# Optimization experiments

Measured on AMD Instinct MI355X. Metric: run time of the kernel, lower is better.

Reference implementation:

```python
import jax, jax.numpy as jnp
import numpy as np

WS = 7       # window_size
SHIFT = 3    # shift_size
HEADS = 3
EPS = 1e-5


def _rel_index():
    # (2, N) coords of a WS x WS window, then pairwise relative offsets -> flat table index
    coords = np.stack(np.meshgrid(np.arange(WS), np.arange(WS), indexing='ij')).reshape(2, -1)
    rel = (coords[:, :, None] - coords[:, None, :]).transpose(1, 2, 0) + (WS - 1)  # (N,N,2)
    return jnp.asarray(rel[..., 0] * (2 * WS - 1) + rel[..., 1])  # (N,N) int


def _layernorm(x, g, b):
    mu = jnp.mean(x, axis=-1, keepdims=True)
    var = jnp.mean(jnp.square(x - mu), axis=-1, keepdims=True)
    return (x - mu) * jax.lax.rsqrt(var + EPS) * g + b


def setup_inputs() -> dict:
    key = jax.random.key(0)
    ks = jax.random.split(key, 6)
    C, HID = 96, 384
    s = 0.02
    return {
        'x': jax.random.normal(ks[0], (8, C, 224, 224), jnp.float32),
        'norm1_g': jnp.ones((C,), jnp.float32),
        'norm1_b': jnp.zeros((C,), jnp.float32),
        'qkv_w': jax.random.normal(ks[1], (C, 3 * C), jnp.float32) * s,
        'qkv_b': jnp.zeros((3 * C,), jnp.float32),
        'proj_w': jax.random.normal(ks[2], (C, C), jnp.float32) * s,
        'proj_b': jnp.zeros((C,), jnp.float32),
        'rel_bias_table': jax.random.normal(ks[3], ((2 * WS - 1) ** 2, HEADS), jnp.float32) * s,
        'norm2_g': jnp.ones((C,), jnp.float32),
        'norm2_b': jnp.zeros((C,), jnp.float32),
        'fc1_w': jax.random.normal(ks[4], (C, HID), jnp.float32) * s,
        'fc1_b': jnp.zeros((HID,), jnp.float32),
        'fc2_w': jax.random.normal(ks[5], (HID, C), jnp.float32) * s,
        'fc2_b': jnp.zeros((C,), jnp.float32),
    }


def reference(x, norm1_g, norm1_b, qkv_w, qkv_b, proj_w, proj_b,
              rel_bias_table, norm2_g, norm2_b, fc1_w, fc1_b, fc2_w, fc2_b):
    B, C, H, W = x.shape
    N = WS * WS
    dh = C // HEADS

    # norm1 over channels (tokens = flattened spatial)
    xt = x.reshape(B, C, H * W).transpose(0, 2, 1)          # (B, L, C)
    xn = _layernorm(xt, norm1_g, norm1_b)
    xs = xn.transpose(0, 2, 1).reshape(B, C, H, W)
    # H, W divisible by WS -> pad is a no-op; cyclic shift
    xs = jnp.roll(xs, (-SHIFT, -SHIFT), axis=(2, 3))

    # window partition -> (B*nW, N, C)
    xw = xs.reshape(B, C, H // WS, WS, W // WS, WS)
    xw = xw.transpose(0, 2, 4, 3, 5, 1).reshape(-1, N, C)

    # window attention with relative position bias (no shift mask, per source)
    Bw = xw.shape[0]
    qkv = (xw @ qkv_w + qkv_b).reshape(Bw, N, 3, HEADS, dh).transpose(2, 0, 3, 1, 4)
    q, k, v = qkv[0], qkv[1], qkv[2]                        # (Bw, h, N, dh)
    attn = jnp.einsum('bhnd,bhmd->bhnm', q, k) * (dh ** -0.5)
    bias = rel_bias_table[_rel_index().reshape(-1)].reshape(N, N, HEADS).transpose(2, 0, 1)
    attn = jax.nn.softmax(attn + bias, axis=-1)
    out = jnp.einsum('bhnm,bhmd->bhnd', attn, v).transpose(0, 2, 1, 3).reshape(Bw, N, C)
    out = out @ proj_w + proj_b

    # window reverse + unshift
    xr = out.reshape(B, H // WS, W // WS, WS, WS, C)
    xr = xr.transpose(0, 5, 1, 3, 2, 4).reshape(B, C, H, W)
    xr = jnp.roll(xr, (SHIFT, SHIFT), axis=(2, 3))

    x = x + xr                                              # residual 1

    # MLP branch with norm2 (exact GELU, matching torch nn.GELU default)
    xt = x.reshape(B, C, H * W).transpose(0, 2, 1)
    xn = _layernorm(xt, norm2_g, norm2_b)
    h = jax.nn.gelu(xn @ fc1_w + fc1_b, approximate=False)
    h = h @ fc2_w + fc2_b
    return x + h.transpose(0, 2, 1).reshape(B, C, H, W)
```

## Files before the change

kernel.cpp:

```cpp
#include <hip/hip_runtime.h>
#include <hip/hip_bf16.h>
#include <math.h>

#define WSZ 7
#define NTOK 49
#define CH 96
#define HIMG 224
#define WIMG 224
#define HWIMG (224*224)
#define SHIFT_ 3
#define HID 384

typedef __attribute__((ext_vector_type(8))) short bf16x8;
typedef __attribute__((ext_vector_type(4))) float f32x4;
typedef unsigned int u32;
typedef unsigned short u16;

__device__ __forceinline__ u32 pk2(float a, float b) {
    u16 ua = __builtin_bit_cast(u16, __float2bfloat16(a));
    u16 ub = __builtin_bit_cast(u16, __float2bfloat16(b));
    return (u32)ua | ((u32)ub << 16);
}
__device__ __forceinline__ float bflo(u32 u) { return __builtin_bit_cast(float, u << 16); }

union FragU { u32 w[4]; bf16x8 v; };

__device__ __forceinline__ bf16x8 regroup(u32 t0w0, u32 t0w1, u32 t1w0, u32 t1w1, int lane) {
    int sl0 = (lane & 15) + ((lane & 16) << 1);
    int sl1 = sl0 + 16;
    u32 x0 = (u32)__shfl((int)t0w0, sl0);
    u32 y0 = (u32)__shfl((int)t1w0, sl0);
    u32 x1 = (u32)__shfl((int)t0w1, sl0);
    u32 y1 = (u32)__shfl((int)t1w1, sl0);
    u32 x2 = (u32)__shfl((int)t0w0, sl1);
    u32 y2 = (u32)__shfl((int)t1w0, sl1);
    u32 x3 = (u32)__shfl((int)t0w1, sl1);
    u32 y3 = (u32)__shfl((int)t1w1, sl1);
    bool lo = lane < 32;
    FragU f;
    f.w[0] = lo ? x0 : y0;
    f.w[1] = lo ? x1 : y1;
    f.w[2] = lo ? x2 : y2;
    f.w[3] = lo ? x3 : y3;
    return f.v;
}

__device__ __forceinline__ float gelu_f(float x) {
    float x2 = x * x;
    float t  = x * (1.5957691216057308f + 0.07135481283587191f * x2);
    float e  = __expf(t);
    float r  = __builtin_amdgcn_rcpf(e + 1.0f);
    return x - x * r;
}

__global__ __launch_bounds__(256) void prep_kernel(
    const float* __restrict__ w1, const float* __restrict__ w2,
    const float* __restrict__ pw, const float* __restrict__ qw,
    __hip_bfloat16* __restrict__ ws, int n)
{
    int i = blockIdx.x * 256 + threadIdx.x;
    if (i >= n) return;
    float val = 0.f;
    if (i < 81920) {
        int ch = i / 20480, r = i - ch * 20480;
        int half = r / 10240;
        int rr = r - half * 10240;
        if (rr < 9984) {
            int row = rr / 104, col = rr - row * 104;
            if (col < 96)
                val = (half == 0) ? w1[col * HID + ch * 96 + row]
                                  : w2[(size_t)(ch * 96 + col) * CH + row];
        }
    } else if (i < 92160) {
        int r = i - 81920;
        if (r < 9984) {
            int row = r / 104, col = r - row * 104;
            if (col < 96) val = pw[col * CH + row];
        }
    } else {
        int j = i - 92160;
        int hh = j / 9984, rr = j - hh * 9984;
        int dp = rr / 104, c = rr - dp * 104;
        if (c < 96) {
            int colW = (dp < 32) ? (hh * 32 + dp)
                     : (dp < 64) ? (96 + hh * 32 + dp - 32)
                                 : (192 + hh * 32 + dp - 64);
            val = qw[c * 288 + colW];
        }
    }
    ws[i] = __float2bfloat16(val);
}

__global__ __launch_bounds__(256) void attn2_kernel(
    const float* __restrict__ x,
    const float* __restrict__ g1, const float* __restrict__ b1,
    const __hip_bfloat16* __restrict__ wsW,
    const float* __restrict__ qkv_b, const float* __restrict__ pb,
    const float* __restrict__ btab,
    __hip_bfloat16* __restrict__ projout)
{
    const int tid  = threadIdx.x;
    const int lane = tid & 63;
    const int wv   = tid >> 6;
    const int l15  = lane & 15;
    const int g    = lane >> 4;
    const int bi   = blockIdx.x;
    const int b    = bi >> 8;
    const int wh   = (bi >> 3) & 31;
    const int ww0  = (bi & 7) * 4;
    const int ww   = ww0 + wv;

    __shared__ float btabL[507];
    __shared__ __align__(16) char uniA[43008];

    __hip_bfloat16 (*xsb)[7][32] = (__hip_bfloat16(*)[7][32])uniA;
    __hip_bfloat16 (*vT)[72] = (__hip_bfloat16(*)[72])(uniA + wv * 4608);
    u32* prS = (u32*)(uniA + wv * 4608);

    for (int idx = tid; idx < 507; idx += 256) btabL[idx] = btab[idx];

    const int colBase = ww0 * 7 + 3;
    const int cA  = colBase & ~3;
    const int cb4 = cA >> 2;
    const int a0  = colBase & 3;
    #pragma unroll
    for (int k = 0; k < 21; ++k) {
        int idx = tid + 256 * k;
        int c = idx / 56, rem = idx - c * 56;
        int r = rem >> 3, cf = rem & 7;
        int gr = wh * 7 + 3 + r; if (gr >= HIMG) gr -= HIMG;
        int g4 = cb4 + cf; if (g4 >= 56) g4 -= 56;
        float4 v = *(const float4*)(x + ((size_t)(b * CH + c) * HIMG + gr) * WIMG + g4 * 4);
        uint2 pk;
        pk.x = pk2(v.x, v.y);
        pk.y = pk2(v.z, v.w);
        *(uint2*)&xsb[c][r][cf * 4] = pk;
    }
    __syncthreads();

    bf16x8 xB[4][3];
    #pragma unroll
    for (int it = 0; it < 4; ++it) {
        int i = it * 16 + l15;
        bool real = i < NTOK;
        int yi = i / 7, xi = i - yi * 7;
        int sc = a0 + wv * 7 + xi;
        float raw[24];
        float s0 = 0.f, s1 = 0.f;
        #pragma unroll
        for (int ks = 0; ks < 3; ++ks)
            #pragma unroll
            for (int t = 0; t < 8; ++t) {
                int c = ks * 32 + g * 8 + t;
                float v = real ? __bfloat162float(xsb[c][yi][sc]) : 0.f;
                raw[ks * 8 + t] = v; s0 += v; s1 += v * v;
            }
        s0 += __shfl_xor(s0, 16); s0 += __shfl_xor(s0, 32);
        s1 += __shfl_xor(s1, 16); s1 += __shfl_xor(s1, 32);
        float mu = s0 * (1.0f / CH);
        float rstd = rsqrtf(s1 * (1.0f / CH) - mu * mu + 1e-5f);
        #pragma unroll
        for (int ks = 0; ks < 3; ++ks)
            #pragma unroll
            for (int t = 0; t < 8; ++t) {
                int c = ks * 32 + g * 8 + t;
                float xv = real ? ((raw[ks * 8 + t] - mu) * rstd * g1[c] + b1[c]) : 0.f;
                xB[it][ks][t] = (short)__builtin_bit_cast(u16, __float2bfloat16(xv));
            }
    }
    __syncthreads();

    const float scale = 0.17677669529663687f;
    bf16x8 aoB[3][4];

    for (int h = 0; h < 3; ++h) {
        const __hip_bfloat16* qkvTg = wsW + 92160 + h * 9984;

        float qb[2][4], kb[2][4], vb[2][4];
        #pragma unroll
        for (int dt = 0; dt < 2; ++dt)
            #pragma unroll
            for (int r = 0; r < 4; ++r) {
                int d = h * 32 + dt * 16 + g * 4 + r;
                qb[dt][r] = qkv_b[d];
                kb[dt][r] = qkv_b[96 + d];
                vb[dt][r] = qkv_b[192 + d];
            }

        u32 Qpk[2][4][2];
        #pragma unroll
        for (int dt = 0; dt < 2; ++dt) {
            const __hip_bfloat16* wr = qkvTg + (dt * 16 + l15) * 104 + g * 8;
            bf16x8 a0f = *(const bf16x8*)(wr);
            bf16x8 a1f = *(const bf16x8*)(wr + 32);
            bf16x8 a2f = *(const bf16x8*)(wr + 64);
            #pragma unroll
            for (int it = 0; it < 4; ++it) {
                f32x4 c4 = {0.f, 0.f, 0.f, 0.f};
                c4 = __builtin_amdgcn_mfma_f32_16x16x32_bf16(a0f, xB[it][0], c4, 0, 0, 0);
                c4 = __builtin_amdgcn_mfma_f32_16x16x32_bf16(a1f, xB[it][1], c4, 0, 0, 0);
                c4 = __builtin_amdgcn_mfma_f32_16x16x32_bf16(a2f, xB[it][2], c4, 0, 0, 0);
                Qpk[dt][it][0] = pk2(c4[0] + qb[dt][0], c4[1] + qb[dt][1]);
                Qpk[dt][it][1] = pk2(c4[2] + qb[dt][2], c4[3] + qb[dt][3]);
            }
        }
        bf16x8 QB[4];
        #pragma unroll
        for (int it = 0; it < 4; ++it)
            QB[it] = regroup(Qpk[0][it][0], Qpk[0][it][1], Qpk[1][it][0], Qpk[1][it][1], lane);

        u32 Kpk[2][4][2];
        #pragma unroll
        for (int dt = 0; dt < 2; ++dt) {
            const __hip_bfloat16* wr = qkvTg + (32 + dt * 16 + l15) * 104 + g * 8;
            bf16x8 a0f = *(const bf16x8*)(wr);
            bf16x8 a1f = *(const bf16x8*)(wr + 32);
            bf16x8 a2f = *(const bf16x8*)(wr + 64);
            #pragma unroll
            for (int it = 0; it < 4; ++it) {
                f32x4 c4 = {0.f, 0.f, 0.f, 0.f};
                c4 = __builtin_amdgcn_mfma_f32_16x16x32_bf16(a0f, xB[it][0], c4, 0, 0, 0);
                c4 = __builtin_amdgcn_mfma_f32_16x16x32_bf16(a1f, xB[it][1], c4, 0, 0, 0);
                c4 = __builtin_amdgcn_mfma_f32_16x16x32_bf16(a2f, xB[it][2], c4, 0, 0, 0);
                Kpk[dt][it][0] = pk2(c4[0] + kb[dt][0], c4[1] + kb[dt][1]);
                Kpk[dt][it][1] = pk2(c4[2] + kb[dt][2], c4[3] + kb[dt][3]);
            }
        }
        bf16x8 KA[4];
        #pragma unroll
        for (int it = 0; it < 4; ++it)
            KA[it] = regroup(Kpk[0][it][0], Kpk[0][it][1], Kpk[1][it][0], Kpk[1][it][1], lane);

        #pragma unroll
        for (int dt = 0; dt < 2; ++dt) {
            const __hip_bfloat16* wr = qkvTg + (64 + dt * 16 + l15) * 104 + g * 8;
            bf16x8 a0f = *(const bf16x8*)(wr);
            bf16x8 a1f = *(const bf16x8*)(wr + 32);
            bf16x8 a2f = *(const bf16x8*)(wr + 64);
            #pragma unroll
            for (int it = 0; it < 4; ++it) {
                f32x4 c4 = {0.f, 0.f, 0.f, 0.f};
                c4 = __builtin_amdgcn_mfma_f32_16x16x32_bf16(a0f, xB[it][0], c4, 0, 0, 0);
                c4 = __builtin_amdgcn_mfma_f32_16x16x32_bf16(a1f, xB[it][1], c4, 0, 0, 0);
                c4 = __builtin_amdgcn_mfma_f32_16x16x32_bf16(a2f, xB[it][2], c4, 0, 0, 0);
                #pragma unroll
                for (int r = 0; r < 4; ++r)
                    vT[dt * 16 + g * 4 + r][it * 16 + l15] = __float2bfloat16(c4[r] + vb[dt][r]);
            }
        }
        bf16x8 VBf[2][2];
        #pragma unroll
        for (int dt = 0; dt < 2; ++dt)
            #pragma unroll
            for (int ks = 0; ks < 2; ++ks)
                VBf[dt][ks] = *(const bf16x8*)&vT[dt * 16 + l15][ks * 32 + g * 8];

        #pragma unroll
        for (int it = 0; it < 4; ++it) {
            f32x4 SC[4];
            #pragma unroll
            for (int jt = 0; jt < 4; ++jt) {
                f32x4 z = {0.f, 0.f, 0.f, 0.f};
                SC[jt] = __builtin_amdgcn_mfma_f32_16x16x32_bf16(KA[jt], QB[it], z, 0, 0, 0);
            }
            int i = it * 16 + l15;
            int yi = i / 7, xi = i - yi * 7;
            float p[16];
            float m = -1e30f;
            #pragma unroll
            for (int jt = 0; jt < 4; ++jt)
                #pragma unroll
                for (int r = 0; r < 4; ++r) {
                    int j = jt * 16 + g * 4 + r;
                    int yj = j / 7, xj = j - yj * 7;
                    int rel = (yi - yj + 6) * 13 + (xi - xj + 6);
                    rel = rel < 0 ? 0 : (rel > 168 ? 168 : rel);
                    float s = (j < NTOK) ? (SC[jt][r] * scale + btabL[rel * 3 + h]) : -1e30f;
                    p[jt * 4 + r] = s;
                    m = fmaxf(m, s);
                }
            m = fmaxf(m, __shfl_xor(m, 16));
            m = fmaxf(m, __shfl_xor(m, 32));
            float sum = 0.f;
            #pragma unroll
            for (int q = 0; q < 16; ++q) { float e = __expf(p[q] - m); p[q] = e; sum += e; }
            sum += __shfl_xor(sum, 16);
            sum += __shfl_xor(sum, 32);
            float inv = 1.f / sum;
            u32 Ppk[4][2];
            #pragma unroll
            for (int jt = 0; jt < 4; ++jt) {
                Ppk[jt][0] = pk2(p[jt * 4 + 0] * inv, p[jt * 4 + 1] * inv);
                Ppk[jt][1] = pk2(p[jt * 4 + 2] * inv, p[jt * 4 + 3] * inv);
            }
            bf16x8 PA0 = regroup(Ppk[0][0], Ppk[0][1], Ppk[1][0], Ppk[1][1], lane);
            bf16x8 PA1 = regroup(Ppk[2][0], Ppk[2][1], Ppk[3][0], Ppk[3][1], lane);
            u32 opk[2][2];
            #pragma unroll
            for (int dt = 0; dt < 2; ++dt) {
                f32x4 o = {0.f, 0.f, 0.f, 0.f};
                o = __builtin_amdgcn_mfma_f32_16x16x32_bf16(PA0, VBf[dt][0], o, 0, 0, 0);
                o = __builtin_amdgcn_mfma_f32_16x16x32_bf16(PA1, VBf[dt][1], o, 0, 0, 0);
                opk[dt][0] = pk2(o[0], o[1]);
                opk[dt][1] = pk2(o[2], o[3]);
            }
            aoB[h][it] = regroup(opk[0][0], opk[0][1], opk[1][0], opk[1][1], lane);
        }
    }

    const __hip_bfloat16* pwTg = wsW + 81920;
    for (int it = 0; it < 4; ++it) {
        #pragma unroll
        for (int mt = 0; mt < 6; ++mt) {
            const __hip_bfloat16* wr = pwTg + (mt * 16 + l15) * 104 + g * 8;
            f32x4 cp = {0.f, 0.f, 0.f, 0.f};
            #pragma unroll
            for (int ks = 0; ks < 3; ++ks) {
                bf16x8 af = *(const bf16x8*)(wr + ks * 32);
                cp = __builtin_amdgcn_mfma_f32_16x16x32_bf16(af, aoB[ks][it], cp, 0, 0, 0);
            }
            float v0 = cp[0] + pb[mt * 16 + g * 4 + 0];
            float v1 = cp[1] + pb[mt * 16 + g * 4 + 1];
            float v2 = cp[2] + pb[mt * 16 + g * 4 + 2];
            float v3 = cp[3] + pb[mt * 16 + g * 4 + 3];
            prS[l15 * 52 + mt * 8 + g * 2 + 0] = pk2(v0, v1);
            prS[l15 * 52 + mt * 8 + g * 2 + 1] = pk2(v2, v3);
        }
        #pragma unroll
        for (int s = 0; s < 3; ++s) {
            int chunk = lane + 64 * s;
            int row = chunk / 12, q = chunk - row * 12;
            int tok = it * 16 + row;
            if (tok < NTOK) {
                int yi = tok / 7, xi = tok - yi * 7;
                int hh = wh * 7 + yi + SHIFT_; if (hh >= HIMG) hh -= HIMG;
                int wp = ww * 7 + xi + SHIFT_; if (wp >= WIMG) wp -= WIMG;
                float4 val = *(const float4*)((const char*)prS + row * 208 + q * 16);
                *(float4*)(projout + ((size_t)b * HWIMG + hh * WIMG + wp) * 96 + q * 8) = val;
            }
        }
    }
}

#define LDSTG(p0, p1, p2, s) { const float4* _s = wsrc + (s) * 1280; \
    p0 = _s[tid]; p1 = _s[tid + 512]; if (tid < 256) p2 = _s[tid + 1024]; }
#define WRSTG(p0, p1, p2, off) { float4* _d = (float4*)(SB + (off)); \
    _d[tid] = p0; _d[tid + 512] = p1; if (tid < 256) _d[tid + 1024] = p2; }

__global__ __launch_bounds__(512, 4) void mlp2_kernel(
    const float* __restrict__ x, const __hip_bfloat16* __restrict__ projout,
    const float* __restrict__ g2, const float* __restrict__ b2,
    const float* __restrict__ bb1, const float* __restrict__ bb2,
    const __hip_bfloat16* __restrict__ wsW,
    float* __restrict__ out)
{
    const int tid = threadIdx.x;
    const int lane = tid & 63, wv = tid >> 6;
    const int l15 = lane & 15, g = lane >> 4;
    const int b = blockIdx.x / 392;
    const int hw0 = (blockIdx.x % 392) * 128;
    const int tok = wv * 16 + l15;

    __shared__ __align__(16) char SB[50688];
    __shared__ float bb1S[HID];

    __hip_bfloat16 (*xnS)[104] = (__hip_bfloat16(*)[104])SB;
    __hip_bfloat16 (*wT0)[104] = (__hip_bfloat16(*)[104])SB;
    __hip_bfloat16 (*wT1)[104] = (__hip_bfloat16(*)[104])(SB + 20480);
    float* ob = (float*)SB;

    const float4* wsrc = (const float4*)wsW;
    float4 ra0, ra1, ra2, rb0, rb1, rb2;

    LDSTG(ra0, ra1, ra2, 0);

    #pragma unroll
    for (int s = 0; s < 3; ++s) {
        int chunk = tid + 512 * s;
        int row = chunk / 12, q = chunk - row * 12;
        *(float4*)&xnS[row][q * 8] =
            *(const float4*)(projout + ((size_t)b * HWIMG + hw0 + row) * 96 + q * 8);
    }
    for (int idx = tid; idx < HID; idx += 512) bb1S[idx] = bb1[idx];
    __syncthreads();

    float xr[24];
    float s0 = 0.f, s1 = 0.f;
    bf16x8 pf[3];
    #pragma unroll
    for (int ks = 0; ks < 3; ++ks)
        pf[ks] = *(const bf16x8*)&xnS[tok][ks * 32 + g * 8];
    const float* xb = x + (size_t)(b * CH) * HWIMG + hw0 + tok;
    #pragma unroll
    for (int ks = 0; ks < 3; ++ks)
        #pragma unroll
        for (int j = 0; j < 8; ++j) {
            int c = ks * 32 + g * 8 + j;
            float xv = xb[(size_t)c * HWIMG];
            float v = xv + bflo((u32)(u16)pf[ks][j]);
            xr[ks * 8 + j] = v; s0 += v; s1 += v * v;
        }
    s0 += __shfl_xor(s0, 16); s0 += __shfl_xor(s0, 32);
    s1 += __shfl_xor(s1, 16); s1 += __shfl_xor(s1, 32);
    float mu = s0 * (1.0f / CH);
    float rstd = rsqrtf(s1 * (1.0f / CH) - mu * mu + 1e-5f);

    bf16x8 xbf[3];
    #pragma unroll
    for (int ks = 0; ks < 3; ++ks) {
        float nv[8];
        #pragma unroll
        for (int j = 0; j < 8; ++j) {
            int c = ks * 32 + g * 8 + j;
            nv[j] = (xr[ks * 8 + j] - mu) * rstd * g2[c] + b2[c];
        }
        FragU f;
        f.w[0] = pk2(nv[0], nv[1]); f.w[1] = pk2(nv[2], nv[3]);
        f.w[2] = pk2(nv[4], nv[5]); f.w[3] = pk2(nv[6], nv[7]);
        xbf[ks] = f.v;
    }
    __syncthreads();

    WRSTG(ra0, ra1, ra2, 0);
    LDSTG(rb0, rb1, rb2, 1);
    __syncthreads();

    f32x4 acc[6];
    #pragma unroll
    for (int mt = 0; mt < 6; ++mt) {
        #pragma unroll
        for (int r = 0; r < 4; ++r) acc[mt][r] = bb2[mt * 16 + g * 4 + r];
    }

    #pragma unroll
    for (int ch = 0; ch < 4; ++ch) {
        u32 hpk[6][2];
        #pragma unroll
        for (int mt = 0; mt < 6; ++mt) {
            f32x4 f = {0.f, 0.f, 0.f, 0.f};
            #pragma unroll
            for (int ks = 0; ks < 3; ++ks) {
                bf16x8 af = *(const bf16x8*)&wT0[mt * 16 + l15][ks * 32 + g * 8];
                f = __builtin_amdgcn_mfma_f32_16x16x32_bf16(af, xbf[ks], f, 0, 0, 0);
            }
            float gl[4];
            #pragma unroll
            for (int r = 0; r < 4; ++r) {
                float a = f[r] + bb1S[ch * 96 + mt * 16 + g * 4 + r];
                gl[r] = gelu_f(a);
            }
            hpk[mt][0] = pk2(gl[0], gl[1]);
            hpk[mt][1] = pk2(gl[2], gl[3]);
        }
        WRSTG(rb0, rb1, rb2, 20480);
        __syncthreads();
        if (ch < 3) LDSTG(ra0, ra1, ra2, 2 * ch + 2);

        bf16x8 hf[3];
        hf[0] = regroup(hpk[0][0], hpk[0][1], hpk[1][0], hpk[1][1], lane);
        hf[1] = regroup(hpk[2][0], hpk[2][1], hpk[3][0], hpk[3][1], lane);
        hf[2] = regroup(hpk[4][0], hpk[4][1], hpk[5][0], hpk[5][1], lane);
        #pragma unroll
        for (int mt = 0; mt < 6; ++mt) {
            #pragma unroll
            for (int ks = 0; ks < 3; ++ks) {
                bf16x8 af = *(const bf16x8*)&wT1[mt * 16 + l15][ks * 32 + g * 8];
                acc[mt] = __builtin_amdgcn_mfma_f32_16x16x32_bf16(af, hf[ks], acc[mt], 0, 0, 0);
            }
        }
        if (ch < 3) WRSTG(ra0, ra1, ra2, 0);
        __syncthreads();
        if (ch < 3) LDSTG(rb0, rb1, rb2, 2 * ch + 3);
    }

    #pragma unroll
    for (int ks = 0; ks < 3; ++ks)
        #pragma unroll
        for (int j = 0; j < 8; ++j)
            ob[tok * 99 + ks * 32 + g * 8 + j] = xr[ks * 8 + j];
    __syncthreads();
    #pragma unroll
    for (int mt = 0; mt < 6; ++mt)
        #pragma unroll
        for (int r = 0; r < 4; ++r)
            ob[tok * 99 + mt * 16 + g * 4 + r] += acc[mt][r];
    __syncthreads();
    #pragma unroll
    for (int k = 0; k < 24; ++k) {
        int idx = tid + 512 * k;
        int c = idx >> 7, t = idx & 127;
        out[(size_t)(b * CH + c) * HWIMG + hw0 + t] = ob[t * 99 + c];
    }
}

__global__ __launch_bounds__(256) void attn_mfma_kernel(
    const float* __restrict__ x,
    const float* __restrict__ g1, const float* __restrict__ b1,
    const float* __restrict__ qkv_w, const float* __restrict__ qkv_b,
    const float* __restrict__ btab,
    float* __restrict__ ao)
{
    const int tid  = threadIdx.x;
    const int lane = tid & 63;
    const int wv   = tid >> 6;
    const int l15  = lane & 15;
    const int g    = lane >> 4;
    const int wid  = blockIdx.x * 4 + wv;
    const int b    = wid >> 10;
    const int wh   = (wid >> 5) & 31;
    const int ww   = wid & 31;

    __shared__ __align__(16) __hip_bfloat16 wT[96][104];
    __shared__ float btabL[507];
    __shared__ __align__(16) __hip_bfloat16 vT[4][32][72];
    __shared__ __align__(16) __hip_bfloat16 Ob[4][64][36];

    int to_h = 0, to_w = 0;
    if (lane < NTOK) {
        int yl = lane / 7, xl = lane - yl * 7;
        to_h = wh * 7 + yl + SHIFT_; if (to_h >= HIMG) to_h -= HIMG;
        to_w = ww * 7 + xl + SHIFT_; if (to_w >= WIMG) to_w -= WIMG;
    }

    bf16x8 xB[4][3];
    #pragma unroll
    for (int it = 0; it < 4; ++it) {
        int i = it * 16 + l15;
        bool real = i < NTOK;
        int yi = i / 7, xi = i - yi * 7;
        int hh = wh * 7 + yi + SHIFT_; if (hh >= HIMG) hh -= HIMG;
        int wp = ww * 7 + xi + SHIFT_; if (wp >= WIMG) wp -= WIMG;
        float raw[24];
        float s0 = 0.f, s1 = 0.f;
        #pragma unroll
        for (int ks = 0; ks < 3; ++ks)
            #pragma unroll
            for (int t = 0; t < 8; ++t) {
                int c = ks * 32 + g * 8 + t;
                float v = real ? x[((size_t)(b * CH + c) * HIMG + hh) * WIMG + wp] : 0.f;
                raw[ks * 8 + t] = v; s0 += v; s1 += v * v;
            }
        s0 += __shfl_xor(s0, 16); s0 += __shfl_xor(s0, 32);
        s1 += __shfl_xor(s1, 16); s1 += __shfl_xor(s1, 32);
        float mu = s0 * (1.0f / CH);
        float rstd = rsqrtf(s1 * (1.0f / CH) - mu * mu + 1e-5f);
        #pragma unroll
        for (int ks = 0; ks < 3; ++ks)
            #pragma unroll
            for (int t = 0; t < 8; ++t) {
                int c = ks * 32 + g * 8 + t;
                float xv = real ? ((raw[ks * 8 + t] - mu) * rstd * g1[c] + b1[c]) : 0.f;
                xB[it][ks][t] = (short)__builtin_bit_cast(u16, __float2bfloat16(xv));
            }
    }

    const float scale = 0.17677669529663687f;

    for (int h = 0; h < 3; ++h) {
        __syncthreads();
        for (int idx = tid; idx < 96 * 96; idx += 256) {
            int c = idx / 96, dp = idx - c * 96;
            int col = (dp < 32) ? (h * 32 + dp) : (dp < 64) ? (96 + h * 32 + dp - 32)
                                                            : (192 + h * 32 + dp - 64);
            wT[dp][c] = __float2bfloat16(qkv_w[c * 288 + col]);
        }
        if (h == 0)
            for (int idx = tid; idx < 507; idx += 256) btabL[idx] = btab[idx];
        __syncthreads();

        float qb[2][4], kb[2][4], vb[2][4];
        #pragma unroll
        for (int dt = 0; dt < 2; ++dt)
            #pragma unroll
            for (int r = 0; r < 4; ++r) {
                int d = h * 32 + dt * 16 + g * 4 + r;
                qb[dt][r] = qkv_b[d];
                kb[dt][r] = qkv_b[96 + d];
                vb[dt][r] = qkv_b[192 + d];
            }

        u32 Qpk[2][4][2];
        #pragma unroll
        for (int dt = 0; dt < 2; ++dt) {
            bf16x8 a0 = *(const bf16x8*)&wT[dt * 16 + l15][0 * 32 + g * 8];
            bf16x8 a1 = *(const bf16x8*)&wT[dt * 16 + l15][1 * 32 + g * 8];
            bf16x8 a2 = *(const bf16x8*)&wT[dt * 16 + l15][2 * 32 + g * 8];
            #pragma unroll
            for (int it = 0; it < 4; ++it) {
                f32x4 c4 = {0.f, 0.f, 0.f, 0.f};
                c4 = __builtin_amdgcn_mfma_f32_16x16x32_bf16(a0, xB[it][0], c4, 0, 0, 0);
                c4 = __builtin_amdgcn_mfma_f32_16x16x32_bf16(a1, xB[it][1], c4, 0, 0, 0);
                c4 = __builtin_amdgcn_mfma_f32_16x16x32_bf16(a2, xB[it][2], c4, 0, 0, 0);
                Qpk[dt][it][0] = pk2(c4[0] + qb[dt][0], c4[1] + qb[dt][1]);
                Qpk[dt][it][1] = pk2(c4[2] + qb[dt][2], c4[3] + qb[dt][3]);
            }
        }
        bf16x8 QB[4];
        #pragma unroll
        for (int it = 0; it < 4; ++it)
            QB[it] = regroup(Qpk[0][it][0], Qpk[0][it][1], Qpk[1][it][0], Qpk[1][it][1], lane);

        u32 Kpk[2][4][2];
        #pragma unroll
        for (int dt = 0; dt < 2; ++dt) {
            bf16x8 a0 = *(const bf16x8*)&wT[32 + dt * 16 + l15][0 * 32 + g * 8];
            bf16x8 a1 = *(const bf16x8*)&wT[32 + dt * 16 + l15][1 * 32 + g * 8];
            bf16x8 a2 = *(const bf16x8*)&wT[32 + dt * 16 + l15][2 * 32 + g * 8];
            #pragma unroll
            for (int it = 0; it < 4; ++it) {
                f32x4 c4 = {0.f, 0.f, 0.f, 0.f};
                c4 = __builtin_amdgcn_mfma_f32_16x16x32_bf16(a0, xB[it][0], c4, 0, 0, 0);
                c4 = __builtin_amdgcn_mfma_f32_16x16x32_bf16(a1, xB[it][1], c4, 0, 0, 0);
                c4 = __builtin_amdgcn_mfma_f32_16x16x32_bf16(a2, xB[it][2], c4, 0, 0, 0);
                Kpk[dt][it][0] = pk2(c4[0] + kb[dt][0], c4[1] + kb[dt][1]);
                Kpk[dt][it][1] = pk2(c4[2] + kb[dt][2], c4[3] + kb[dt][3]);
            }
        }
        bf16x8 KA[4];
        #pragma unroll
        for (int it = 0; it < 4; ++it)
            KA[it] = regroup(Kpk[0][it][0], Kpk[0][it][1], Kpk[1][it][0], Kpk[1][it][1], lane);

        #pragma unroll
        for (int dt = 0; dt < 2; ++dt) {
            bf16x8 a0 = *(const bf16x8*)&wT[64 + dt * 16 + l15][0 * 32 + g * 8];
            bf16x8 a1 = *(const bf16x8*)&wT[64 + dt * 16 + l15][1 * 32 + g * 8];
            bf16x8 a2 = *(const bf16x8*)&wT[64 + dt * 16 + l15][2 * 32 + g * 8];
            #pragma unroll
            for (int it = 0; it < 4; ++it) {
                f32x4 c4 = {0.f, 0.f, 0.f, 0.f};
                c4 = __builtin_amdgcn_mfma_f32_16x16x32_bf16(a0, xB[it][0], c4, 0, 0, 0);
                c4 = __builtin_amdgcn_mfma_f32_16x16x32_bf16(a1, xB[it][1], c4, 0, 0, 0);
                c4 = __builtin_amdgcn_mfma_f32_16x16x32_bf16(a2, xB[it][2], c4, 0, 0, 0);
                #pragma unroll
                for (int r = 0; r < 4; ++r)
                    vT[wv][dt * 16 + g * 4 + r][it * 16 + l15] = __float2bfloat16(c4[r] + vb[dt][r]);
            }
        }
        bf16x8 VBf[2][2];
        #pragma unroll
        for (int dt = 0; dt < 2; ++dt)
            #pragma unroll
            for (int ks = 0; ks < 2; ++ks)
                VBf[dt][ks] = *(const bf16x8*)&vT[wv][dt * 16 + l15][ks * 32 + g * 8];

        #pragma unroll
        for (int it = 0; it < 4; ++it) {
            f32x4 SC[4];
            #pragma unroll
            for (int jt = 0; jt < 4; ++jt) {
                f32x4 z = {0.f, 0.f, 0.f, 0.f};
                SC[jt] = __builtin_amdgcn_mfma_f32_16x16x32_bf16(KA[jt], QB[it], z, 0, 0, 0);
            }
            int i = it * 16 + l15;
            int yi = i / 7, xi = i - yi * 7;
            float p[16];
            float m = -1e30f;
            #pragma unroll
            for (int jt = 0; jt < 4; ++jt)
                #pragma unroll
                for (int r = 0; r < 4; ++r) {
                    int j = jt * 16 + g * 4 + r;
                    int yj = j / 7, xj = j - yj * 7;
                    int rel = (yi - yj + 6) * 13 + (xi - xj + 6);
                    rel = rel < 0 ? 0 : (rel > 168 ? 168 : rel);
                    float s = (j < NTOK) ? (SC[jt][r] * scale + btabL[rel * 3 + h]) : -1e30f;
                    p[jt * 4 + r] = s;
                    m = fmaxf(m, s);
                }
            m = fmaxf(m, __shfl_xor(m, 16));
            m = fmaxf(m, __shfl_xor(m, 32));
            float sum = 0.f;
            #pragma unroll
            for (int q = 0; q < 16; ++q) { float e = __expf(p[q] - m); p[q] = e; sum += e; }
            sum += __shfl_xor(sum, 16);
            sum += __shfl_xor(sum, 32);
            float inv = 1.f / sum;
            u32 Ppk[4][2];
            #pragma unroll
            for (int jt = 0; jt < 4; ++jt) {
                Ppk[jt][0] = pk2(p[jt * 4 + 0] * inv, p[jt * 4 + 1] * inv);
                Ppk[jt][1] = pk2(p[jt * 4 + 2] * inv, p[jt * 4 + 3] * inv);
            }
            bf16x8 PA0 = regroup(Ppk[0][0], Ppk[0][1], Ppk[1][0], Ppk[1][1], lane);
            bf16x8 PA1 = regroup(Ppk[2][0], Ppk[2][1], Ppk[3][0], Ppk[3][1], lane);
            #pragma unroll
            for (int dt = 0; dt < 2; ++dt) {
                f32x4 o = {0.f, 0.f, 0.f, 0.f};
                o = __builtin_amdgcn_mfma_f32_16x16x32_bf16(PA0, VBf[dt][0], o, 0, 0, 0);
                o = __builtin_amdgcn_mfma_f32_16x16x32_bf16(PA1, VBf[dt][1], o, 0, 0, 0);
                #pragma unroll
                for (int r = 0; r < 4; ++r)
                    Ob[wv][it * 16 + g * 4 + r][dt * 16 + l15] = __float2bfloat16(o[r]);
            }
        }

        if (lane < NTOK) {
            #pragma unroll 8
            for (int ch = 0; ch < 32; ++ch)
                ao[((size_t)(b * CH + h * 32 + ch) * HIMG + to_h) * WIMG + to_w] =
                    __bfloat162float(Ob[wv][lane][ch]);
        }
    }
}

__global__ __launch_bounds__(512, 4) void fuse2_kernel(
    const float* __restrict__ x, const float* ao,
    const float* __restrict__ pw, const float* __restrict__ pb,
    const float* __restrict__ g2, const float* __restrict__ b2,
    const float* __restrict__ w1, const float* __restrict__ bb1,
    const float* __restrict__ w2, const float* __restrict__ bb2,
    const __hip_bfloat16* __restrict__ wsW, int useWs,
    float* out)
{
    const int tid = threadIdx.x;
    const int lane = tid & 63, wv = tid >> 6;
    const int l15 = lane & 15, g = lane >> 4;
    const int b = blockIdx.x / 392;
    const int hw0 = (blockIdx.x % 392) * 128;
    const int m0 = wv * 16;
    const int t = tid & 127;
    const int c0 = tid >> 7;

    __shared__ __align__(16) char WREG[46592];
    __shared__ __align__(16) __hip_bfloat16 xnS[128][104];
    __shared__ float part0[4][128], part1[4][128];
    __shared__ float muS[128], rsS[128];
    __shared__ float bb1S[HID];

    __hip_bfloat16 (*pwT)[104]   = (__hip_bfloat16(*)[104])WREG;
    __hip_bfloat16 (*projS)[104] = (__hip_bfloat16(*)[104])(WREG + 19968);
    __hip_bfloat16 (*w1T)[104]   = (__hip_bfloat16(*)[104])WREG;
    __hip_bfloat16 (*w2T)[104]   = (__hip_bfloat16(*)[104])(WREG + 20480);
    __hip_bfloat16 (*obuf)[104]  = (__hip_bfloat16(*)[104])WREG;

    float xreg[24];

    for (int idx = tid, k = 0; idx < 96 * 128; idx += 512, ++k) {
        int c = idx >> 7, tt = idx & 127;
        size_t gi = (size_t)(b * CH + c) * HWIMG + hw0 + tt;
        xreg[k] = x[gi];
        xnS[tt][c] = __float2bfloat16(ao[gi]);
    }
    if (useWs) {
        const float4* src = (const float4*)wsW + 10240;
        float4* dst = (float4*)WREG;
        for (int i = tid; i < 1280; i += 512) dst[i] = src[i];
    } else {
        for (int idx = tid; idx < 96 * 96; idx += 512) {
            int c = idx / 96, oc = idx - c * 96;
            pwT[oc][c] = __float2bfloat16(pw[c * 96 + oc]);
        }
    }
    for (int idx = tid; idx < HID; idx += 512) bb1S[idx] = bb1[idx];
    __syncthreads();

    {
        bf16x8 bfr[3];
        #pragma unroll
        for (int ks = 0; ks < 3; ++ks)
            bfr[ks] = *(const bf16x8*)&xnS[m0 + l15][ks * 32 + g * 8];
        #pragma unroll
        for (int mt = 0; mt < 6; ++mt) {
            f32x4 cp = {0.f, 0.f, 0.f, 0.f};
            #pragma unroll
            for (int ks = 0; ks < 3; ++ks) {
                bf16x8 af = *(const bf16x8*)&pwT[mt * 16 + l15][ks * 32 + g * 8];
                cp = __builtin_amdgcn_mfma_f32_16x16x32_bf16(af, bfr[ks], cp, 0, 0, 0);
            }
            #pragma unroll
            for (int r = 0; r < 4; ++r) {
                int oc = mt * 16 + g * 4 + r;
                projS[m0 + l15][oc] = __float2bfloat16(cp[r] + pb[oc]);
            }
        }
    }
    __syncthreads();

    {
        float s0 = 0.f, s1 = 0.f;
        #pragma unroll
        for (int k = 0; k < 24; ++k) {
            int c = c0 + 4 * k;
            float v = xreg[k] + __bfloat162float(projS[t][c]);
            xreg[k] = v; s0 += v; s1 += v * v;
        }
        part0[c0][t] = s0; part1[c0][t] = s1;
    }
    __syncthreads();
    if (tid < 128) {
        float s0 = part0[0][tid] + part0[1][tid] + part0[2][tid] + part0[3][tid];
        float s1 = part1[0][tid] + part1[1][tid] + part1[2][tid] + part1[3][tid];
        float m = s0 * (1.0f / CH);
        muS[tid] = m;
        rsS[tid] = rsqrtf(s1 * (1.0f / CH) - m * m + 1e-5f);
    }
    __syncthreads();
    #pragma unroll
    for (int k = 0; k < 24; ++k) {
        int c = c0 + 4 * k;
        xnS[t][c] = __float2bfloat16((xreg[k] - muS[t]) * rsS[t] * g2[c] + b2[c]);
    }
    __syncthreads();

    bf16x8 xbf[3];
    #pragma unroll
    for (int ks = 0; ks < 3; ++ks)
        xbf[ks] = *(const bf16x8*)&xnS[m0 + l15][ks * 32 + g * 8];

    f32x4 acc[6];
    #pragma unroll
    for (int mt = 0; mt < 6; ++mt)
        #pragma unroll
        for (int r = 0; r < 4; ++r)
            acc[mt][r] = bb2[mt * 16 + g * 4 + r];

    for (int ch = 0; ch < 4; ++ch) {
        if (useWs) {
            const float4* src = (const float4*)wsW + (size_t)ch * 2560;
            float4* dst = (float4*)WREG;
            #pragma unroll
            for (int i = tid; i < 2560; i += 512) dst[i] = src[i];
        } else {
            for (int idx = tid; idx < 2 * 96 * 96; idx += 512) {
                if (idx < 9216) {
                    int kk = idx / 96, n = idx - kk * 96;
                    w1T[n][kk] = __float2bfloat16(w1[kk * HID + ch * 96 + n]);
                } else {
                    int j = idx - 9216;
                    int kk = j / 96, n = j - kk * 96;
                    w2T[n][kk] = __float2bfloat16(w2[(size_t)(ch * 96 + kk) * CH + n]);
                }
            }
        }
        __syncthreads();

        u32 hpk[6][2];
        #pragma unroll
        for (int mt = 0; mt < 6; ++mt) {
            f32x4 f = {0.f, 0.f, 0.f, 0.f};
            #pragma unroll
            for (int ks = 0; ks < 3; ++ks) {
                bf16x8 af = *(const bf16x8*)&w1T[mt * 16 + l15][ks * 32 + g * 8];
                f = __builtin_amdgcn_mfma_f32_16x16x32_bf16(af, xbf[ks], f, 0, 0, 0);
            }
            float gl[4];
            #pragma unroll
            for (int r = 0; r < 4; ++r) {
                float a = f[r] + bb1S[ch * 96 + mt * 16 + g * 4 + r];
                gl[r] = gelu_f(a);
            }
            hpk[mt][0] = pk2(gl[0], gl[1]);
            hpk[mt][1] = pk2(gl[2], gl[3]);
        }
        bf16x8 hf[3];
        hf[0] = regroup(hpk[0][0], hpk[0][1], hpk[1][0], hpk[1][1], lane);
        hf[1] = regroup(hpk[2][0], hpk[2][1], hpk[3][0], hpk[3][1], lane);
        hf[2] = regroup(hpk[4][0], hpk[4][1], hpk[5][0], hpk[5][1], lane);

        #pragma unroll
        for (int mt = 0; mt < 6; ++mt)
            #pragma unroll
            for (int ks = 0; ks < 3; ++ks) {
                bf16x8 af = *(const bf16x8*)&w2T[mt * 16 + l15][ks * 32 + g * 8];
                acc[mt] = __builtin_amdgcn_mfma_f32_16x16x32_bf16(af, hf[ks], acc[mt], 0, 0, 0);
            }
        __syncthreads();
    }

    #pragma unroll
    for (int mt = 0; mt < 6; ++mt)
        #pragma unroll
        for (int r = 0; r < 4; ++r)
            obuf[m0 + l15][mt * 16 + g * 4 + r] = __float2bfloat16(acc[mt][r]);
    __syncthreads();
    #pragma unroll
    for (int k = 0; k < 24; ++k) {
        int c = c0 + 4 * k;
        out[(size_t)(b * CH + c) * HWIMG + hw0 + t] = xreg[k] + __bfloat162float(obuf[t][c]);
    }
}

extern "C" void kernel_launch(void* const* d_in, const int* in_sizes, int n_in,
                              void* d_out, int out_size, void* d_ws, size_t ws_size,
                              hipStream_t stream) {
    const float* x    = (const float*)d_in[0];
    const float* n1g  = (const float*)d_in[1];
    const float* n1b  = (const float*)d_in[2];
    const float* qkvw = (const float*)d_in[3];
    const float* qkvb = (const float*)d_in[4];
    const float* pw   = (const float*)d_in[5];
    const float* pbv  = (const float*)d_in[6];
    const float* bt   = (const float*)d_in[7];
    const float* n2g  = (const float*)d_in[8];
    const float* n2b  = (const float*)d_in[9];
    const float* f1w  = (const float*)d_in[10];
    const float* f1b  = (const float*)d_in[11];
    const float* f2w  = (const float*)d_in[12];
    const float* f2b  = (const float*)d_in[13];
    float* out = (float*)d_out;

    const size_t FULL_NEED = 262144ull + 77070336ull;
    if (ws_size >= FULL_NEED) {
        __hip_bfloat16* wsW = (__hip_bfloat16*)d_ws;
        __hip_bfloat16* projout = (__hip_bfloat16*)((char*)d_ws + 262144);
        prep_kernel<<<477, 256, 0, stream>>>(f1w, f2w, pw, qkvw, wsW, 122112);
        attn2_kernel<<<2048, 256, 0, stream>>>(x, n1g, n1b, wsW, qkvb, pbv, bt, projout);
        mlp2_kernel<<<3136, 512, 0, stream>>>(x, projout, n2g, n2b, f1b, f2b, wsW, out);
    } else {
        int useWs = (ws_size >= 184320) ? 1 : 0;
        if (useWs)
            prep_kernel<<<360, 256, 0, stream>>>(f1w, f2w, pw, qkvw, (__hip_bfloat16*)d_ws, 92160);
        attn_mfma_kernel<<<2048, 256, 0, stream>>>(x, n1g, n1b, qkvw, qkvb, bt, out);
        fuse2_kernel<<<3136, 512, 0, stream>>>(x, out, pw, pbv, n2g, n2b, f1w, f1b, f2w, f2b,
                                               (const __hip_bfloat16*)d_ws, useWs, out);
    }
}
```

Baseline: 405.5 us.

## Stage input in 32-channel slabs to cut LDS and precompute bias indices

Input staging into shared memory now goes through a 32-channel slab, loaded three times in sequence, instead of holding all 96 channels at once. This shrinks LDS use so that, together with launch_bounds(256,4), more blocks can be resident per CU. LayerNorm statistics are accumulated across the slabs, and normalization is applied afterwards to packed bf16 fragments using vectorized gamma/beta loads. Relative-position bias indexing is simplified by precomputing packed per-lane token offsets and padding the bias table with -1e30 sentinels, which removes divisions and masking from the softmax loop. The cost is extra barriers and a small extra rounding step, since raw values are stored as bf16 before normalization.

Measured after the change: 477.1 us. +17.7%, slower.

```diff
diff --git a/kernel.cpp b/kernel.cpp
--- a/kernel.cpp
+++ b/kernel.cpp
@@ -22,6 +22,7 @@
     return (u32)ua | ((u32)ub << 16);
 }
 __device__ __forceinline__ float bflo(u32 u) { return __builtin_bit_cast(float, u << 16); }
+__device__ __forceinline__ float bfhi(u32 u) { return __builtin_bit_cast(float, u & 0xFFFF0000u); }
 
 union FragU { u32 w[4]; bf16x8 v; };
 
@@ -91,7 +92,7 @@
     ws[i] = __float2bfloat16(val);
 }
 
-__global__ __launch_bounds__(256) void attn2_kernel(
+__global__ __launch_bounds__(256, 4) void attn2_kernel(
     const float* __restrict__ x,
     const float* __restrict__ g1, const float* __restrict__ b1,
     const __hip_bfloat16* __restrict__ wsW,
@@ -110,65 +111,108 @@
     const int ww0  = (bi & 7) * 4;
     const int ww   = ww0 + wv;
 
-    __shared__ float btabL[507];
-    __shared__ __align__(16) char uniA[43008];
-
-    __hip_bfloat16 (*xsb)[7][32] = (__hip_bfloat16(*)[7][32])uniA;
-    __hip_bfloat16 (*vT)[72] = (__hip_bfloat16(*)[72])(uniA + wv * 4608);
-    u32* prS = (u32*)(uniA + wv * 4608);
-
-    for (int idx = tid; idx < 507; idx += 256) btabL[idx] = btab[idx];
+    __shared__ float btabL[512];
+    __shared__ __align__(16) __hip_bfloat16 slab[32][7][32];
+    __shared__ __align__(16) char uniA[4][4608];
+
+    __hip_bfloat16 (*vT)[72] = (__hip_bfloat16(*)[72])uniA[wv];
+    u32* prS = (u32*)uniA[wv];
+
+    for (int idx = tid; idx < 510; idx += 256)
+        btabL[idx] = (idx < 507) ? btab[idx] : -1e30f;
 
     const int colBase = ww0 * 7 + 3;
-    const int cA  = colBase & ~3;
-    const int cb4 = cA >> 2;
+    const int cb4 = (colBase & ~3) >> 2;
     const int a0  = colBase & 3;
-    #pragma unroll
-    for (int k = 0; k < 21; ++k) {
-        int idx = tid + 256 * k;
-        int c = idx / 56, rem = idx - c * 56;
-        int r = rem >> 3, cf = rem & 7;
-        int gr = wh * 7 + 3 + r; if (gr >= HIMG) gr -= HIMG;
-        int g4 = cb4 + cf; if (g4 >= 56) g4 -= 56;
-        float4 v = *(const float4*)(x + ((size_t)(b * CH + c) * HIMG + gr) * WIMG + g4 * 4);
-        uint2 pk;
-        pk.x = pk2(v.x, v.y);
-        pk.y = pk2(v.z, v.w);
-        *(uint2*)&xsb[c][r][cf * 4] = pk;
-    }
-    __syncthreads();
-
-    bf16x8 xB[4][3];
+
+    int yiA[4], scA[4], base4[4]; bool realA[4];
     #pragma unroll
     for (int it = 0; it < 4; ++it) {
         int i = it * 16 + l15;
-        bool real = i < NTOK;
-        int yi = i / 7, xi = i - yi * 7;
-        int sc = a0 + wv * 7 + xi;
-        float raw[24];
-        float s0 = 0.f, s1 = 0.f;
-        #pragma unroll
-        for (int ks = 0; ks < 3; ++ks)
+        realA[it] = i < NTOK;
+        int yi = (i * 37) >> 8; int xi = i - yi * 7;
+        yiA[it] = yi; scA[it] = a0 + wv * 7 + xi;
+        base4[it] = (yi + 6) * 13 + (xi + 6);
+    }
+
+    u32 jo4[4];
+    #pragma unroll
+    for (int jt = 0; jt < 4; ++jt) {
+        u32 pack = 0;
+        #pragma unroll
+        for (int r = 0; r < 4; ++r) {
+            int j = jt * 16 + g * 4 + r;
+            int yj = (j * 37) >> 8; int xj = j - yj * 7;
+            int jov = (j < NTOK) ? (yj * 13 + xj) : -128;
+            pack |= ((u32)(jov & 255)) << (8 * r);
+        }
+        jo4[jt] = pack;
+    }
+
+    float s0a[4] = {0.f, 0.f, 0.f, 0.f}, s1a[4] = {0.f, 0.f, 0.f, 0.f};
+    FragU xf[4][3];
+
+    for (int ks = 0; ks < 3; ++ks) {
+        #pragma unroll
+        for (int k = 0; k < 7; ++k) {
+            int idx = tid + 256 * k;
+            int c = idx / 56, rem = idx - c * 56;
+            int r = rem >> 3, cf = rem & 7;
+            int gr = wh * 7 + 3 + r; if (gr >= HIMG) gr -= HIMG;
+            int g4 = cb4 + cf; if (g4 >= 56) g4 -= 56;
+            float4 v = *(const float4*)(x + ((size_t)(b * CH + ks * 32 + c) * HIMG + gr) * WIMG + g4 * 4);
+            uint2 pk;
+            pk.x = pk2(v.x, v.y);
+            pk.y = pk2(v.z, v.w);
+            *(uint2*)&slab[c][r][cf * 4] = pk;
+        }
+        __syncthreads();
+        #pragma unroll
+        for (int it = 0; it < 4; ++it) {
+            float v[8];
             #pragma unroll
             for (int t = 0; t < 8; ++t) {
-                int c = ks * 32 + g * 8 + t;
-                float v = real ? __bfloat162float(xsb[c][yi][sc]) : 0.f;
-                raw[ks * 8 + t] = v; s0 += v; s1 += v * v;
-            }
-        s0 += __shfl_xor(s0, 16); s0 += __shfl_xor(s0, 32);
-        s1 += __shfl_xor(s1, 16); s1 += __shfl_xor(s1, 32);
+                float val = realA[it] ? __bfloat162float(slab[g * 8 + t][yiA[it]][scA[it]]) : 0.f;
+                v[t] = val;
+                s0a[it] += val; s1a[it] += val * val;
+            }
+            xf[it][ks].w[0] = pk2(v[0], v[1]);
+            xf[it][ks].w[1] = pk2(v[2], v[3]);
+            xf[it][ks].w[2] = pk2(v[4], v[5]);
+            xf[it][ks].w[3] = pk2(v[6], v[7]);
+        }
+        __syncthreads();
+    }
+
+    float mu4[4], rs4[4];
+    #pragma unroll
+    for (int it = 0; it < 4; ++it) {
+        float s0 = s0a[it]; s0 += __shfl_xor(s0, 16); s0 += __shfl_xor(s0, 32);
+        float s1 = s1a[it]; s1 += __shfl_xor(s1, 16); s1 += __shfl_xor(s1, 32);
         float mu = s0 * (1.0f / CH);
-        float rstd = rsqrtf(s1 * (1.0f / CH) - mu * mu + 1e-5f);
-        #pragma unroll
-        for (int ks = 0; ks < 3; ++ks)
-            #pragma unroll
-            for (int t = 0; t < 8; ++t) {
-                int c = ks * 32 + g * 8 + t;
-                float xv = real ? ((raw[ks * 8 + t] - mu) * rstd * g1[c] + b1[c]) : 0.f;
-                xB[it][ks][t] = (short)__builtin_bit_cast(u16, __float2bfloat16(xv));
-            }
-    }
-    __syncthreads();
+        mu4[it] = mu;
+        rs4[it] = rsqrtf(s1 * (1.0f / CH) - mu * mu + 1e-5f);
+    }
+    #pragma unroll
+    for (int ks = 0; ks < 3; ++ks) {
+        float4 gA = *(const float4*)&g1[ks * 32 + g * 8];
+        float4 gB = *(const float4*)&g1[ks * 32 + g * 8 + 4];
+        float4 bA = *(const float4*)&b1[ks * 32 + g * 8];
+        float4 bB = *(const float4*)&b1[ks * 32 + g * 8 + 4];
+        float gg[8] = {gA.x, gA.y, gA.z, gA.w, gB.x, gB.y, gB.z, gB.w};
+        float bb[8] = {bA.x, bA.y, bA.z, bA.w, bB.x, bB.y, bB.z, bB.w};
+        #pragma unroll
+        for (int it = 0; it < 4; ++it) {
+            #pragma unroll
+            for (int w = 0; w < 4; ++w) {
+                u32 u = xf[it][ks].w[w];
+                float lo = bflo(u), hi = bfhi(u);
+                float nlo = realA[it] ? ((lo - mu4[it]) * rs4[it] * gg[2 * w]     + bb[2 * w])     : 0.f;
+                float nhi = realA[it] ? ((hi - mu4[it]) * rs4[it] * gg[2 * w + 1] + bb[2 * w + 1]) : 0.f;
+                xf[it][ks].w[w] = pk2(nlo, nhi);
+            }
+        }
+    }
 
     const float scale = 0.17677669529663687f;
     bf16x8 aoB[3][4];
@@ -197,9 +241,9 @@
             #pragma unroll
             for (int it = 0; it < 4; ++it) {
                 f32x4 c4 = {0.f, 0.f, 0.f, 0.f};
-                c4 = __builtin_amdgcn_mfma_f32_16x16x32_bf16(a0f, xB[it][0], c4, 0, 0, 0);
-                c4 = __builtin_amdgcn_mfma_f32_16x16x32_bf16(a1f, xB[it][1], c4, 0, 0, 0);
-                c4 = __builtin_amdgcn_mfma_f32_16x16x32_bf16(a2f, xB[it][2], c4, 0, 0, 0);
+                c4 = __builtin_amdgcn_mfma_f32_16x16x32_bf16(a0f, xf[it][0].v, c4, 0, 0, 0);
+                c4 = __builtin_amdgcn_mfma_f32_16x16x32_bf16(a1f, xf[it][1].v, c4, 0, 0, 0);
+                c4 = __builtin_amdgcn_mfma_f32_16x16x32_bf16(a2f, xf[it][2].v, c4, 0, 0, 0);
                 Qpk[dt][it][0] = pk2(c4[0] + qb[dt][0], c4[1] + qb[dt][1]);
                 Qpk[dt][it][1] = pk2(c4[2] + qb[dt][2], c4[3] + qb[dt][3]);
             }
@@ -219,9 +263,9 @@
             #pragma unroll
             for (int it = 0; it < 4; ++it) {
                 f32x4 c4 = {0.f, 0.f, 0.f, 0.f};
-                c4 = __builtin_amdgcn_mfma_f32_16x16x32_bf16(a0f, xB[it][0], c4, 0, 0, 0);
-                c4 = __builtin_amdgcn_mfma_f32_16x16x32_bf16(a1f, xB[it][1], c4, 0, 0, 0);
-                c4 = __builtin_amdgcn_mfma_f32_16x16x32_bf16(a2f, xB[it][2], c4, 0, 0, 0);
+                c4 = __builtin_amdgcn_mfma_f32_16x16x32_bf16(a0f, xf[it][0].v, c4, 0, 0, 0);
+                c4 = __builtin_amdgcn_mfma_f32_16x16x32_bf16(a1f, xf[it][1].v, c4, 0, 0, 0);
+                c4 = __builtin_amdgcn_mfma_f32_16x16x32_bf16(a2f, xf[it][2].v, c4, 0, 0, 0);
                 Kpk[dt][it][0] = pk2(c4[0] + kb[dt][0], c4[1] + kb[dt][1]);
                 Kpk[dt][it][1] = pk2(c4[2] + kb[dt][2], c4[3] + kb[dt][3]);
             }
@@ -240,9 +284,9 @@
             #pragma unroll
             for (int it = 0; it < 4; ++it) {
                 f32x4 c4 = {0.f, 0.f, 0.f, 0.f};
-                c4 = __builtin_amdgcn_mfma_f32_16x16x32_bf16(a0f, xB[it][0], c4, 0, 0, 0);
-                c4 = __builtin_amdgcn_mfma_f32_16x16x32_bf16(a1f, xB[it][1], c4, 0, 0, 0);
-                c4 = __builtin_amdgcn_mfma_f32_16x16x32_bf16(a2f, xB[it][2], c4, 0, 0, 0);
+                c4 = __builtin_amdgcn_mfma_f32_16x16x32_bf16(a0f, xf[it][0].v, c4, 0, 0, 0);
+                c4 = __builtin_amdgcn_mfma_f32_16x16x32_bf16(a1f, xf[it][1].v, c4, 0, 0, 0);
+                c4 = __builtin_amdgcn_mfma_f32_16x16x32_bf16(a2f, xf[it][2].v, c4, 0, 0, 0);
                 #pragma unroll
                 for (int r = 0; r < 4; ++r)
                     vT[dt * 16 + g * 4 + r][it * 16 + l15] = __float2bfloat16(c4[r] + vb[dt][r]);
@@ -263,19 +307,18 @@
                 f32x4 z = {0.f, 0.f, 0.f, 0.f};
                 SC[jt] = __builtin_amdgcn_mfma_f32_16x16x32_bf16(KA[jt], QB[it], z, 0, 0, 0);
             }
-            int i = it * 16 + l15;
-            int yi = i / 7, xi = i - yi * 7;
+            const int basei = base4[it];
             float p[16];
             float m = -1e30f;
             #pragma unroll
             for (int jt = 0; jt < 4; ++jt)
                 #pragma unroll
                 for (int r = 0; r < 4; ++r) {
-                    int j = jt * 16 + g * 4 + r;
-                    int yj = j / 7, xj = j - yj * 7;
-                    int rel = (yi - yj + 6) * 13 + (xi - xj + 6);
-                    rel = rel < 0 ? 0 : (rel > 168 ? 168 : rel);
-                    float s = (j < NTOK) ? (SC[jt][r] * scale + btabL[rel * 3 + h]) : -1e30f;
+                    int jov = ((int)(jo4[jt] << ((3 - r) * 8))) >> 24;
+                    int idx = basei - jov;
+                    idx = idx < 0 ? 0 : idx;
+                    idx = idx > 169 ? 169 : idx;
+                    float s = fmaf(SC[jt][r], scale, btabL[idx * 3 + h]);
                     p[jt * 4 + r] = s;
                     m = fmaxf(m, s);
                 }
```
